# Optimization experiments

Measured on AMD Instinct MI355X. Metric: run time of the kernel, lower is better.

## Reference

```python
import jax, jax.numpy as jnp
import numpy as np

# Model config (mirrors Kitnet after initialization):
INPUT_SIZE = 1000
M = 10                 # max_autoencoder_size -> features per cluster
N_CLUSTERS = INPUT_SIZE // M   # 100 tiny autoencoders
HIDDEN_RATIO = 0.5
H_SMALL = max(3, int(M * HIDDEN_RATIO))          # 5
H_META = max(3, int(N_CLUSTERS * HIDDEN_RATIO))  # 50
BATCH = 65536


def setup_inputs() -> dict:
    key = jax.random.key(0)
    ks = jax.random.split(key, 8)
    x = jax.random.normal(ks[0], (BATCH, INPUT_SIZE), dtype=jnp.float32)
    # cluster feature indices: a random permutation of features split into
    # N_CLUSTERS groups of M (equal-size clusters, faithful to gather pattern)
    perm = jax.random.permutation(ks[1], INPUT_SIZE)
    feat_idx = perm.reshape(N_CLUSTERS, M).astype(jnp.int32)
    # per-cluster AE params (PyTorch Linear default init ~ U(-1/sqrt(fan_in),..))
    def lin_init(k, shape, fan_in):
        b = 1.0 / np.sqrt(fan_in)
        return jax.random.uniform(k, shape, minval=-b, maxval=b, dtype=jnp.float32)
    W_enc = lin_init(ks[2], (N_CLUSTERS, M, H_SMALL), M)
    b_enc = lin_init(ks[3], (N_CLUSTERS, H_SMALL), M)
    W_dec = lin_init(ks[4], (N_CLUSTERS, H_SMALL, M), H_SMALL)
    b_dec = lin_init(ks[5], (N_CLUSTERS, M), H_SMALL)
    # meta autoencoder params
    We1 = lin_init(ks[6], (N_CLUSTERS, H_META), N_CLUSTERS)
    k7, k8, k9 = jax.random.split(ks[7], 3)
    be1 = lin_init(k7, (H_META,), N_CLUSTERS)
    Wd1 = lin_init(k8, (H_META, N_CLUSTERS), H_META)
    bd1 = lin_init(k9, (N_CLUSTERS,), H_META)
    return {"x": x, "feat_idx": feat_idx,
            "W_enc": W_enc, "b_enc": b_enc, "W_dec": W_dec, "b_dec": b_dec,
            "We1": We1, "be1": be1, "Wd1": Wd1, "bd1": bd1}


def reference(x, feat_idx, W_enc, b_enc, W_dec, b_dec, We1, be1, Wd1, bd1):
    # gather per-cluster features: [B, C, M]
    xg = x[:, feat_idx]
    # encoder: relu(xg @ W_enc + b_enc) -> [B, C, H]
    h = jax.nn.relu(jnp.einsum('bcm,cmh->bch', xg, W_enc) + b_enc)
    # decoder -> [B, C, M]
    rec = jnp.einsum('bch,chm->bcm', h, W_dec) + b_dec
    # per-cluster RMSE -> [B, C]
    err = jnp.sqrt(jnp.mean((xg - rec) ** 2, axis=-1))
    # meta autoencoder over reconstruction errors
    hm = jax.nn.relu(err @ We1 + be1)
    err_rec = hm @ Wd1 + bd1
    final_error = jnp.sqrt(jnp.mean((err - err_rec) ** 2, axis=-1))
    return jax.nn.sigmoid(final_error)
```

## Files before the change

kernel.cpp:

```cpp
#include <hip/hip_runtime.h>
#include <stdint.h>

typedef _Float16 h2 __attribute__((ext_vector_type(2)));

#define N_CLUSTERS 100
#define M 10
#define HS 5
#define HM 50
#define GROUP 64
#define NWAVE 16
#define XPITCH_B 2004

#define O_WE1T 0
#define O_WD1T 5200
#define O_HMT  15600
#define O_PART 22000
#define O_LWE  128256
#define O_LWD  138656
#define O_ERR  150656
#define LDS_TOTAL 163456

__device__ __forceinline__ float fdot2(uint32_t a, uint32_t b, float c) {
    return __builtin_amdgcn_fdot2(__builtin_bit_cast(h2, a),
                                  __builtin_bit_cast(h2, b), c, false);
}
__device__ __forceinline__ uint32_t pk2(float a, float b) {
    return __builtin_bit_cast(uint32_t, __builtin_amdgcn_cvt_pkrtz(a, b));
}
__device__ __forceinline__ float h2f(unsigned short u) {
    return (float)__builtin_bit_cast(_Float16, u);
}

__global__ void __launch_bounds__(1024) kitnet_kernel(
    const float* __restrict__ x,
    const int*   __restrict__ fi,
    const float* __restrict__ W_enc, const float* __restrict__ b_enc,
    const float* __restrict__ W_dec, const float* __restrict__ b_dec,
    const float* __restrict__ We1,   const float* __restrict__ be1,
    const float* __restrict__ Wd1,   const float* __restrict__ bd1,
    float* __restrict__ out)
{
    extern __shared__ char smem[];
    const int tid  = threadIdx.x;
    const int lane = tid & 63;
    const int w    = __builtin_amdgcn_readfirstlane(tid >> 6);
    const int b0   = blockIdx.x * GROUP;

    uint32_t* lweU = (uint32_t*)(smem + O_LWE);
    uint32_t* lwdU = (uint32_t*)(smem + O_LWD);
    unsigned short* errL = (unsigned short*)(smem + O_ERR);

    const float4* xr = (const float4*)(x + (size_t)b0 * 1000);
    for (int i = tid; i < 16000; i += 1024) {
        float4 v = xr[i];
        int row = i / 250;
        int c4  = i - row * 250;
        uint32_t* p = (uint32_t*)(smem + row * XPITCH_B + c4 * 8);
        p[0] = pk2(v.x, v.y);
        p[1] = pk2(v.z, v.w);
    }
    for (int i = tid; i < 2500; i += 1024) {
        int c = i / 25, r = i - c * 25;
        int k = r / 5, pp = r - k * 5;
        lweU[c * 26 + r] = pk2(W_enc[c * 50 + (2 * pp) * 5 + k],
                               W_enc[c * 50 + (2 * pp + 1) * 5 + k]);
    }
    for (int i = tid; i < 3000; i += 1024) {
        int c = i / 30, r = i - c * 30;
        int m = r / 3, q = r - m * 3;
        float lo = W_dec[c * 50 + (2 * q) * 10 + m];
        float hi = (q == 2) ? 0.f : W_dec[c * 50 + (2 * q + 1) * 10 + m];
        lwdU[c * 30 + r] = pk2(lo, hi);
    }
    __syncthreads();

    const unsigned short* myrow = (const unsigned short*)(smem + lane * XPITCH_B);
    auto do_cluster = [&](int c) {
        int cols[M];
        #pragma unroll
        for (int m = 0; m < M; ++m) cols[m] = fi[c * 10 + m];
        uint32_t xpk[5];
        #pragma unroll
        for (int p = 0; p < 5; ++p)
            xpk[p] = (uint32_t)myrow[cols[2 * p]] |
                     ((uint32_t)myrow[cols[2 * p + 1]] << 16);
        const uint2* eW = (const uint2*)(lweU + c * 26);
        uint32_t wreg[25];
        #pragma unroll
        for (int q = 0; q < 12; ++q) { uint2 t = eW[q]; wreg[2*q] = t.x; wreg[2*q+1] = t.y; }
        wreg[24] = (lweU + c * 26)[24];
        float h[HS];
        #pragma unroll
        for (int k = 0; k < HS; ++k) h[k] = b_enc[c * 5 + k];
        #pragma unroll
        for (int k = 0; k < HS; ++k) {
            #pragma unroll
            for (int p = 0; p < 5; ++p)
                h[k] = fdot2(xpk[p], wreg[k * 5 + p], h[k]);
        }
        uint32_t hp[3];
        hp[0] = pk2(fmaxf(h[0], 0.f), fmaxf(h[1], 0.f));
        hp[1] = pk2(fmaxf(h[2], 0.f), fmaxf(h[3], 0.f));
        hp[2] = pk2(fmaxf(h[4], 0.f), 0.f);
        const uint2* dW = (const uint2*)(lwdU + c * 30);
        uint32_t dreg[30];
        #pragma unroll
        for (int q = 0; q < 15; ++q) { uint2 t = dW[q]; dreg[2*q] = t.x; dreg[2*q+1] = t.y; }
        float acc = 0.f;
        #pragma unroll
        for (int m = 0; m < M; ++m) {
            float r = b_dec[c * 10 + m];
            r = fdot2(hp[0], dreg[m * 3 + 0], r);
            r = fdot2(hp[1], dreg[m * 3 + 1], r);
            r = fdot2(hp[2], dreg[m * 3 + 2], r);
            h2 xv = __builtin_bit_cast(h2, xpk[m >> 1]);
            float xf = (float)((m & 1) ? xv.y : xv.x);
            float d = xf - r;
            acc = __builtin_fmaf(d, d, acc);
        }
        _Float16 ev = (_Float16)__builtin_sqrtf(acc * 0.1f);
        errL[lane * 100 + c] = __builtin_bit_cast(unsigned short, ev);
    };
    #pragma unroll 2
    for (int t = 0; t < 6; ++t) do_cluster(w + 16 * t);
    if (w < 4) do_cluster(w + 96);
    __syncthreads();

    uint32_t* we1U = (uint32_t*)(smem + O_WE1T);
    uint32_t* wd1U = (uint32_t*)(smem + O_WD1T);
    for (int i = tid; i < 1250; i += 1024) {
        int j = i / 25, cp = i - j * 25;
        we1U[j * 26 + cp] = pk2(We1[(2 * cp) * 50 + j], We1[(2 * cp + 1) * 50 + j]);
    }
    for (int i = tid; i < 2500; i += 1024) {
        int c = i / 25, jp = i - c * 25;
        wd1U[c * 26 + jp] = pk2(Wd1[(2 * jp) * 100 + c], Wd1[(2 * jp + 1) * 100 + c]);
    }
    __syncthreads();

    uint32_t* hmp = (uint32_t*)(smem + O_HMT);
    const uint2* e2 = (const uint2*)(errL + lane * 100);
    auto do_pair = [&](int p) {
        const int j0 = 2 * p;
        float a0 = be1[j0], a1 = be1[j0 + 1];
        const uint2* w0 = (const uint2*)(we1U + j0 * 26);
        const uint2* w1 = (const uint2*)(we1U + (j0 + 1) * 26);
        #pragma unroll
        for (int ch = 0; ch < 12; ++ch) {
            uint2 e = e2[ch]; uint2 wa = w0[ch]; uint2 wb = w1[ch];
            a0 = fdot2(e.x, wa.x, a0); a0 = fdot2(e.y, wa.y, a0);
            a1 = fdot2(e.x, wb.x, a1); a1 = fdot2(e.y, wb.y, a1);
        }
        uint32_t et = ((const uint32_t*)e2)[24];
        a0 = fdot2(et, (we1U + j0 * 26)[24], a0);
        a1 = fdot2(et, (we1U + (j0 + 1) * 26)[24], a1);
        hmp[p * 64 + lane] = pk2(fmaxf(a0, 0.f), fmaxf(a1, 0.f));
    };
    do_pair(w);
    if (w < 9) do_pair(w + 16);
    __syncthreads();

    uint32_t hmreg[25];
    #pragma unroll
    for (int p = 0; p < 25; ++p) hmreg[p] = hmp[p * 64 + lane];
    float facc = 0.f;
    auto do_dec = [&](int c) {
        float er = h2f(errL[lane * 100 + c]);
        float r = bd1[c];
        const uint2* wr = (const uint2*)(wd1U + c * 26);
        #pragma unroll
        for (int q = 0; q < 12; ++q) {
            uint2 t = wr[q];
            r = fdot2(hmreg[2 * q], t.x, r);
            r = fdot2(hmreg[2 * q + 1], t.y, r);
        }
        r = fdot2(hmreg[24], (wd1U + c * 26)[24], r);
        float d = er - r;
        facc = __builtin_fmaf(d, d, facc);
    };
    #pragma unroll 2
    for (int t = 0; t < 6; ++t) do_dec(w + 16 * t);
    if (w < 4) do_dec(w + 96);

    float* part = (float*)(smem + O_PART);
    part[w * 64 + lane] = facc;
    __syncthreads();
    if (tid < 64) {
        float s = 0.f;
        #pragma unroll
        for (int i = 0; i < NWAVE; ++i) s += part[i * 64 + tid];
        float fe = __builtin_sqrtf(s * 0.01f);
        out[b0 + tid] = 1.f / (1.f + __expf(-fe));
    }
}

extern "C" void kernel_launch(void* const* d_in, const int* in_sizes, int n_in,
                              void* d_out, int out_size, void* d_ws, size_t ws_size,
                              hipStream_t stream) {
    const float* x     = (const float*)d_in[0];
    const int*   fi    = (const int*)  d_in[1];
    const float* W_enc = (const float*)d_in[2];
    const float* b_enc = (const float*)d_in[3];
    const float* W_dec = (const float*)d_in[4];
    const float* b_dec = (const float*)d_in[5];
    const float* We1   = (const float*)d_in[6];
    const float* be1   = (const float*)d_in[7];
    const float* Wd1   = (const float*)d_in[8];
    const float* bd1   = (const float*)d_in[9];
    float* out = (float*)d_out;

    (void)hipFuncSetAttribute((const void*)kitnet_kernel,
                              hipFuncAttributeMaxDynamicSharedMemorySize, LDS_TOTAL);
    kitnet_kernel<<<65536 / GROUP, 1024, LDS_TOTAL, stream>>>(
        x, fi, W_enc, b_enc, W_dec, b_dec, We1, be1, Wd1, bd1, out);
}
```

Before: 435.9 us.

## Make blocks persistent over four row tiles with register-prefetched x loads

Each block now processes four 64-row tiles instead of one, cutting the grid to 256 blocks. The next tile's x rows are loaded into registers (16 float4 per thread) during the meta-autoencoder phase and written to LDS after the current tile finishes. This is meant to overlap global loads with compute and amortize the per-cluster weight setup. The costs are extra register pressure, more barriers per tile, and only 256 blocks at 1024 threads each, which may underfill the GPU. The meta weights are still re-staged every tile.

```diff
diff --git a/kernel.cpp b/kernel.cpp
--- a/kernel.cpp
+++ b/kernel.cpp
@@ -8,6 +8,7 @@
 #define HS 5
 #define HM 50
 #define GROUP 64
+#define TILES 4
 #define NWAVE 16
 #define XPITCH_B 2004
 
@@ -44,21 +45,37 @@
     const int tid  = threadIdx.x;
     const int lane = tid & 63;
     const int w    = __builtin_amdgcn_readfirstlane(tid >> 6);
-    const int b0   = blockIdx.x * GROUP;
 
     uint32_t* lweU = (uint32_t*)(smem + O_LWE);
     uint32_t* lwdU = (uint32_t*)(smem + O_LWD);
     unsigned short* errL = (unsigned short*)(smem + O_ERR);
 
-    const float4* xr = (const float4*)(x + (size_t)b0 * 1000);
-    for (int i = tid; i < 16000; i += 1024) {
-        float4 v = xr[i];
-        int row = i / 250;
-        int c4  = i - row * 250;
-        uint32_t* p = (uint32_t*)(smem + row * XPITCH_B + c4 * 8);
-        p[0] = pk2(v.x, v.y);
-        p[1] = pk2(v.z, v.w);
-    }
+    auto load_x = [&](float4 (&vb)[16], int row0) {
+        const float4* xr = (const float4*)(x + (size_t)row0 * 1000);
+        #pragma unroll
+        for (int k = 0; k < 16; ++k) {
+            int i = tid + (k << 10);
+            if (i < 16000) vb[k] = xr[i];
+        }
+    };
+    auto write_x = [&](float4 (&vb)[16]) {
+        #pragma unroll
+        for (int k = 0; k < 16; ++k) {
+            int i = tid + (k << 10);
+            if (i < 16000) {
+                int row = i / 250;
+                int c4  = i - row * 250;
+                uint32_t* p = (uint32_t*)(smem + row * XPITCH_B + c4 * 8);
+                p[0] = pk2(vb[k].x, vb[k].y);
+                p[1] = pk2(vb[k].z, vb[k].w);
+            }
+        }
+    };
+
+    const int rowbase = blockIdx.x * (GROUP * TILES);
+
+    float4 vbuf[16];
+    load_x(vbuf, rowbase);
     for (int i = tid; i < 2500; i += 1024) {
         int c = i / 25, r = i - c * 25;
         int k = r / 5, pp = r - k * 5;
@@ -72,6 +89,7 @@
         float hi = (q == 2) ? 0.f : W_dec[c * 50 + (2 * q + 1) * 10 + m];
         lwdU[c * 30 + r] = pk2(lo, hi);
     }
+    write_x(vbuf);
     __syncthreads();
 
     const unsigned short* myrow = (const unsigned short*)(smem + lane * XPITCH_B);
@@ -121,24 +139,11 @@
         _Float16 ev = (_Float16)__builtin_sqrtf(acc * 0.1f);
         errL[lane * 100 + c] = __builtin_bit_cast(unsigned short, ev);
     };
-    #pragma unroll 2
-    for (int t = 0; t < 6; ++t) do_cluster(w + 16 * t);
-    if (w < 4) do_cluster(w + 96);
-    __syncthreads();
 
     uint32_t* we1U = (uint32_t*)(smem + O_WE1T);
     uint32_t* wd1U = (uint32_t*)(smem + O_WD1T);
-    for (int i = tid; i < 1250; i += 1024) {
-        int j = i / 25, cp = i - j * 25;
-        we1U[j * 26 + cp] = pk2(We1[(2 * cp) * 50 + j], We1[(2 * cp + 1) * 50 + j]);
-    }
-    for (int i = tid; i < 2500; i += 1024) {
-        int c = i / 25, jp = i - c * 25;
-        wd1U[c * 26 + jp] = pk2(Wd1[(2 * jp) * 100 + c], Wd1[(2 * jp + 1) * 100 + c]);
-    }
-    __syncthreads();
-
-    uint32_t* hmp = (uint32_t*)(smem + O_HMT);
+    uint32_t* hmp  = (uint32_t*)(smem + O_HMT);
+    float*    part = (float*)(smem + O_PART);
     const uint2* e2 = (const uint2*)(errL + lane * 100);
     auto do_pair = [&](int p) {
         const int j0 = 2 * p;
@@ -156,41 +161,67 @@
         a1 = fdot2(et, (we1U + (j0 + 1) * 26)[24], a1);
         hmp[p * 64 + lane] = pk2(fmaxf(a0, 0.f), fmaxf(a1, 0.f));
     };
-    do_pair(w);
-    if (w < 9) do_pair(w + 16);
-    __syncthreads();
-
-    uint32_t hmreg[25];
-    #pragma unroll
-    for (int p = 0; p < 25; ++p) hmreg[p] = hmp[p * 64 + lane];
-    float facc = 0.f;
-    auto do_dec = [&](int c) {
-        float er = h2f(errL[lane * 100 + c]);
-        float r = bd1[c];
-        const uint2* wr = (const uint2*)(wd1U + c * 26);
-        #pragma unroll
-        for (int q = 0; q < 12; ++q) {
-            uint2 t = wr[q];
-            r = fdot2(hmreg[2 * q], t.x, r);
-            r = fdot2(hmreg[2 * q + 1], t.y, r);
-        }
-        r = fdot2(hmreg[24], (wd1U + c * 26)[24], r);
-        float d = er - r;
-        facc = __builtin_fmaf(d, d, facc);
-    };
-    #pragma unroll 2
-    for (int t = 0; t < 6; ++t) do_dec(w + 16 * t);
-    if (w < 4) do_dec(w + 96);
-
-    float* part = (float*)(smem + O_PART);
-    part[w * 64 + lane] = facc;
-    __syncthreads();
-    if (tid < 64) {
-        float s = 0.f;
-        #pragma unroll
-        for (int i = 0; i < NWAVE; ++i) s += part[i * 64 + tid];
-        float fe = __builtin_sqrtf(s * 0.01f);
-        out[b0 + tid] = 1.f / (1.f + __expf(-fe));
+
+    #pragma unroll 1
+    for (int t = 0; t < TILES; ++t) {
+        const int b0t = rowbase + t * GROUP;
+
+        #pragma unroll 2
+        for (int u = 0; u < 6; ++u) do_cluster(w + 16 * u);
+        if (w < 4) do_cluster(w + 96);
+        __syncthreads();
+
+        if (t + 1 < TILES) load_x(vbuf, b0t + GROUP);
+
+        for (int i = tid; i < 1250; i += 1024) {
+            int j = i / 25, cp = i - j * 25;
+            we1U[j * 26 + cp] = pk2(We1[(2 * cp) * 50 + j], We1[(2 * cp + 1) * 50 + j]);
+        }
+        for (int i = tid; i < 2500; i += 1024) {
+            int c = i / 25, jp = i - c * 25;
+            wd1U[c * 26 + jp] = pk2(Wd1[(2 * jp) * 100 + c], Wd1[(2 * jp + 1) * 100 + c]);
+        }
+        __syncthreads();
+
+        do_pair(w);
+        if (w < 9) do_pair(w + 16);
+        __syncthreads();
+
+        uint32_t hmreg[25];
+        #pragma unroll
+        for (int p = 0; p < 25; ++p) hmreg[p] = hmp[p * 64 + lane];
+        float facc = 0.f;
+        auto do_dec = [&](int c) {
+            float er = h2f(errL[lane * 100 + c]);
+            float r = bd1[c];
+            const uint2* wr = (const uint2*)(wd1U + c * 26);
+            #pragma unroll
+            for (int q = 0; q < 12; ++q) {
+                uint2 tt = wr[q];
+                r = fdot2(hmreg[2 * q], tt.x, r);
+                r = fdot2(hmreg[2 * q + 1], tt.y, r);
+            }
+            r = fdot2(hmreg[24], (wd1U + c * 26)[24], r);
+            float d = er - r;
+            facc = __builtin_fmaf(d, d, facc);
+        };
+        #pragma unroll 2
+        for (int u = 0; u < 6; ++u) do_dec(w + 16 * u);
+        if (w < 4) do_dec(w + 96);
+        part[w * 64 + lane] = facc;
+        __syncthreads();
+
+        if (tid < 64) {
+            float s = 0.f;
+            #pragma unroll
+            for (int i = 0; i < NWAVE; ++i) s += part[i * 64 + tid];
+            float fe = __builtin_sqrtf(s * 0.01f);
+            out[b0t + tid] = 1.f / (1.f + __expf(-fe));
+        }
+        __syncthreads();
+
+        if (t + 1 < TILES) write_x(vbuf);
+        __syncthreads();
     }
 }
 
@@ -211,6 +242,6 @@
 
     (void)hipFuncSetAttribute((const void*)kitnet_kernel,
                               hipFuncAttributeMaxDynamicSharedMemorySize, LDS_TOTAL);
-    kitnet_kernel<<<65536 / GROUP, 1024, LDS_TOTAL, stream>>>(
+    kitnet_kernel<<<65536 / (GROUP * TILES), 1024, LDS_TOTAL, stream>>>(
         x, fi, W_enc, b_enc, W_dec, b_dec, We1, be1, Wd1, bd1, out);
 }
```

Result: no change. 433.8 us (-0.5%).
